# Kernel tuning notes

Measured on AMD Instinct MI355X. Metric: run time of the kernel, lower is better.

## Reference

```python
import jax, jax.numpy as jnp
import numpy as np
from jax import lax

T, K, D = 2097152, 8, 4
LOG_2PI = float(np.log(2.0 * np.pi))


def setup_inputs() -> dict:
    key = jax.random.key(0)
    k1, k2, k3, k4 = jax.random.split(key, 4)
    return {
        "x_seq": jax.random.normal(k1, (T, D), dtype=jnp.float32),
        "unnormalized_trans": jax.random.normal(k2, (K, K), dtype=jnp.float32),
        "unnormalized_pi": jax.random.normal(k3, (K,), dtype=jnp.float32),
        "means": jax.random.normal(k4, (K, D), dtype=jnp.float32) * 0.01,
        "log_std": jnp.zeros((K, D), dtype=jnp.float32),
    }


def reference(x_seq, unnormalized_trans, unnormalized_pi, means, log_std):
    # Row-stochastic transition / initial distributions in log space
    log_trans = jax.nn.log_softmax(unnormalized_trans, axis=-1)  # [K, K]
    log_pi = jax.nn.log_softmax(unnormalized_pi, axis=-1)        # [K]

    # Diagonal-Gaussian log emission densities: [T, K]
    std = jnp.exp(log_std)                                        # [K, D]
    z = (x_seq[:, None, :] - means[None, :, :]) / std[None, :, :]  # [T, K, D]
    log_em = jnp.sum(-0.5 * LOG_2PI - log_std[None] - 0.5 * z * z, axis=-1)  # [T, K]

    # Forward algorithm in log space (strictly sequential recurrence)
    alpha0 = log_pi + log_em[0]  # [K]

    def step(alpha, em_t):
        # alpha[i] + log_trans[i, j], logsumexp over source state i
        alpha = em_t + jax.scipy.special.logsumexp(alpha[:, None] + log_trans, axis=0)
        return alpha, None

    alpha, _ = lax.scan(step, alpha0, log_em[1:])
    return jax.scipy.special.logsumexp(alpha, axis=0)
```

## Files before the change

### kernel.cpp

```cpp
#include <hip/hip_runtime.h>
#include <math.h>

#define T_LEN 2097152
#define K 8
#define D 4
#define CHUNK 8
#define TPB 256
#define NBLK (T_LEN / (CHUNK * TPB))
#define MS4 19
#define NMID 8

typedef float f2 __attribute__((ext_vector_type(2)));

__device__ __forceinline__ f2 fma2(f2 a, f2 b, f2 c) { return __builtin_elementwise_fma(a, b, c); }
__device__ __forceinline__ f2 max2(f2 a, f2 b) { return __builtin_elementwise_max(a, b); }
__device__ __forceinline__ f2 splat(float s) { f2 r; r.x = s; r.y = s; return r; }


__device__ __forceinline__ float4* matp4(float* lm, int li) {
    return reinterpret_cast<float4*>(lm) + li * MS4 + ((li >> 1) & 3);
}

__device__ __forceinline__ void renorm2(f2 M[K][4], float& shift) {
    f2 m2 = max2(max2(M[0][0], M[0][1]), max2(M[0][2], M[0][3]));
#pragma unroll
    for (int i = 1; i < K; ++i)
        m2 = max2(m2, max2(max2(M[i][0], M[i][1]), max2(M[i][2], M[i][3])));
    float mx = fmaxf(m2.x, m2.y);
    int ex = (__float_as_int(mx) >> 23) & 255;
    float scale = __int_as_float((254 - ex) << 23);
    shift += (float)(ex - 127);
    f2 sc = splat(scale);
#pragma unroll
    for (int i = 0; i < K; ++i)
#pragma unroll
        for (int jj = 0; jj < 4; ++jj) M[i][jj] = M[i][jj] * sc;
}

__device__ __forceinline__ void store_mat(float* lm, int li, const f2 M[K][4]) {
    float4* dst = matp4(lm, li);
#pragma unroll
    for (int i = 0; i < K; ++i) {
        float4 w0, w1;
        w0.x = M[i][0].x; w0.y = M[i][0].y; w0.z = M[i][1].x; w0.w = M[i][1].y;
        w1.x = M[i][2].x; w1.y = M[i][2].y; w1.z = M[i][3].x; w1.w = M[i][3].y;
        dst[i * 2] = w0;
        dst[i * 2 + 1] = w1;
    }
}

__device__ __forceinline__ void combine8(float* lm, float* lsh, int li, int ri, int i) {
    const float4* Lb = matp4(lm, li);
    const float4* Rb = matp4(lm, ri);
    float4 la = Lb[i * 2], lb = Lb[i * 2 + 1];
    float4 R[16];
#pragma unroll
    for (int q = 0; q < 16; ++q) R[q] = Rb[q];
    float lk[8] = {la.x, la.y, la.z, la.w, lb.x, lb.y, lb.z, lb.w};
    f2 acc[4];
#pragma unroll
    for (int k = 0; k < 8; ++k) {
        f2 s = splat(lk[k]);
        f2 r0, r1, r2_, r3;
        r0.x = R[2 * k].x;     r0.y = R[2 * k].y;
        r1.x = R[2 * k].z;     r1.y = R[2 * k].w;
        r2_.x = R[2 * k + 1].x; r2_.y = R[2 * k + 1].y;
        r3.x = R[2 * k + 1].z;  r3.y = R[2 * k + 1].w;
        if (k == 0) {
            acc[0] = s * r0; acc[1] = s * r1; acc[2] = s * r2_; acc[3] = s * r3;
        } else {
            acc[0] = fma2(s, r0, acc[0]); acc[1] = fma2(s, r1, acc[1]);
            acc[2] = fma2(s, r2_, acc[2]); acc[3] = fma2(s, r3, acc[3]);
        }
    }
    f2 m2 = max2(max2(acc[0], acc[1]), max2(acc[2], acc[3]));
    float mx = fmaxf(m2.x, m2.y);
    mx = fmaxf(mx, __shfl_xor(mx, 1));
    mx = fmaxf(mx, __shfl_xor(mx, 2));
    mx = fmaxf(mx, __shfl_xor(mx, 4));
    int ex = (__float_as_int(mx) >> 23) & 255;
    float scale = __int_as_float((254 - ex) << 23);
    float ns = lsh[li] + lsh[ri] + (float)(ex - 127);
    f2 sc = splat(scale);
    f2 o0 = acc[0] * sc, o1 = acc[1] * sc, o2 = acc[2] * sc, o3 = acc[3] * sc;
    float4 w0, w1;
    w0.x = o0.x; w0.y = o0.y; w0.z = o1.x; w0.w = o1.y;
    w1.x = o2.x; w1.y = o2.y; w1.z = o3.x; w1.w = o3.y;
    float4* Ob = matp4(lm, li);
    Ob[i * 2] = w0;
    Ob[i * 2 + 1] = w1;
    if (i == 0) lsh[li] = ns;
}

__device__ __forceinline__ void tree_levels(float* lm, float* lsh) {
    const int g = threadIdx.x >> 3;
    const int i = threadIdx.x & 7;
#pragma unroll 1
    for (int lvl = 1; lvl <= 3; ++lvl) {
        const int c = 64 >> (lvl - 1);
        const int S = 1 << (lvl - 1);
#pragma unroll 1
        for (int m = g; m < c; m += 32) combine8(lm, lsh, 2 * m * S, 2 * m * S + S, i);
        __syncthreads();
    }
    if (threadIdx.x < 64) {
#pragma unroll 1
        for (int lvl = 4; lvl <= 7; ++lvl) {
            const int c = 64 >> (lvl - 1);
            const int S = 1 << (lvl - 1);
            if (g < c) combine8(lm, lsh, 2 * g * S, 2 * g * S + S, i);
            asm volatile("s_waitcnt lgkmcnt(0)" ::: "memory");
        }
    }
}

__device__ __forceinline__ void hybrid_tree(f2 P2[K][4], float shift, float* lm, float* lsh) {
    const int t = threadIdx.x;
    if ((t & 1) == 0) {
        store_mat(lm, t >> 1, P2);
        lsh[t >> 1] = shift;
    }
    __syncthreads();
    if (t & 1) {
        const float4* src = matp4(lm, t >> 1);
        float lsv = lsh[t >> 1];
        f2 C[K][4];
#pragma unroll
        for (int i = 0; i < K; ++i) {
            float4 la = src[i * 2], lb = src[i * 2 + 1];
            float lk[8] = {la.x, la.y, la.z, la.w, lb.x, lb.y, lb.z, lb.w};
            f2 q[4];
#pragma unroll
            for (int k = 0; k < 8; ++k) {
                f2 s = splat(lk[k]);
                if (k == 0) {
#pragma unroll
                    for (int jj = 0; jj < 4; ++jj) q[jj] = s * P2[k][jj];
                } else {
#pragma unroll
                    for (int jj = 0; jj < 4; ++jj) q[jj] = fma2(s, P2[k][jj], q[jj]);
                }
            }
#pragma unroll
            for (int jj = 0; jj < 4; ++jj) C[i][jj] = q[jj];
        }
        float ns = shift + lsv;
        renorm2(C, ns);
        store_mat(lm, t >> 1, C);
        lsh[t >> 1] = ns;
    }
    __syncthreads();
    tree_levels(lm, lsh);
}

__device__ __forceinline__ float emit_e2(const f2 ca2[4], const f2 cb2[4][4],
                                         const f2 cc2[4][4], float4 x, f2 e2[4]) {
    f2 x0 = splat(x.x), x1 = splat(x.y), x2 = splat(x.z), x3 = splat(x.w);
    f2 em2[4];
#pragma unroll
    for (int jj = 0; jj < 4; ++jj) {
        f2 t = ca2[jj];
        t = fma2(fma2(cc2[0][jj], x0, cb2[0][jj]), x0, t);
        t = fma2(fma2(cc2[1][jj], x1, cb2[1][jj]), x1, t);
        t = fma2(fma2(cc2[2][jj], x2, cb2[2][jj]), x2, t);
        t = fma2(fma2(cc2[3][jj], x3, cb2[3][jj]), x3, t);
        em2[jj] = t;
    }
    f2 m2 = max2(max2(em2[0], em2[1]), max2(em2[2], em2[3]));
    float me = fmaxf(m2.x, m2.y);
#pragma unroll
    for (int jj = 0; jj < 4; ++jj) {
        e2[jj].x = exp2f(em2[jj].x - me);
        e2[jj].y = exp2f(em2[jj].y - me);
    }
    return me;
}

__global__ void hmm_setup(const float* __restrict__ x,
                          const float* __restrict__ ut,
                          const float* __restrict__ up,
                          const float* __restrict__ mn,
                          const float* __restrict__ lsd,
                          float* __restrict__ ws) {
    const int lane = threadIdx.x;
    const float L2PI = 1.83787706640934548356f;
    const float LOG2E = 1.44269504088896340736f;

    float v = ut[lane];
    float m = v;
    m = fmaxf(m, __shfl_xor(m, 1));
    m = fmaxf(m, __shfl_xor(m, 2));
    m = fmaxf(m, __shfl_xor(m, 4));
    float e = expf(v - m);
    float s = e;
    s += __shfl_xor(s, 1); s += __shfl_xor(s, 2); s += __shfl_xor(s, 4);
    ws[lane] = e / s;

    float pv = up[lane & 7];
    float pm = pv;
    pm = fmaxf(pm, __shfl_xor(pm, 1));
    pm = fmaxf(pm, __shfl_xor(pm, 2));
    pm = fmaxf(pm, __shfl_xor(pm, 4));
    float pe = expf(pv - pm);
    float ps = pe;
    ps += __shfl_xor(ps, 1); ps += __shfl_xor(ps, 2); ps += __shfl_xor(ps, 4);
    float pival = pe / ps;

    int k = (lane & 31) >> 2, d = lane & 3;
    float lv = lsd[k * D + d];
    float mu = mn[k * D + d];
    float iv = expf(-2.f * lv);
    float bn = mu * iv;
    float cn = -0.5f * iv;
    float aterm = -0.5f * L2PI - lv - 0.5f * mu * mu * iv;
    float ak = aterm;
    ak += __shfl_xor(ak, 1); ak += __shfl_xor(ak, 2);
    if (lane < 32) {
        ws[72 + lane]  = bn * LOG2E;
        ws[104 + lane] = cn * LOG2E;
        if (d == 0) ws[64 + k] = ak * LOG2E;
    }

    float xd = x[d];
    float part = (cn * xd + bn) * xd + aterm;
    part += __shfl_xor(part, 1); part += __shfl_xor(part, 2);
    float pik = __shfl(pival, k);
    if (lane < 32 && d == 0) ws[136 + k] = pik * expf(part);
}

__global__ __launch_bounds__(TPB) void hmm_main(const float* __restrict__ x,
                                                const float* __restrict__ cst,
                                                float* __restrict__ bp,
                                                float* __restrict__ bs) {
    __shared__ __align__(16) float lm[128 * 76];
    __shared__ float lsh[128];
    const int tid = blockIdx.x * TPB + threadIdx.x;

    float Tr[K][K];
#pragma unroll
    for (int i = 0; i < K; ++i)
#pragma unroll
        for (int j = 0; j < K; ++j) Tr[i][j] = cst[i * K + j];
    f2 Tr2[K][4];
#pragma unroll
    for (int i = 0; i < K; ++i)
#pragma unroll
        for (int jj = 0; jj < 4; ++jj) { Tr2[i][jj].x = Tr[i][2 * jj]; Tr2[i][jj].y = Tr[i][2 * jj + 1]; }

    f2 ca2[4], cb2[4][4], cc2[4][4];
#pragma unroll
    for (int jj = 0; jj < 4; ++jj) {
        ca2[jj].x = cst[64 + 2 * jj]; ca2[jj].y = cst[64 + 2 * jj + 1];
#pragma unroll
        for (int d = 0; d < 4; ++d) {
            cb2[d][jj].x = cst[72 + (2 * jj) * 4 + d];  cb2[d][jj].y = cst[72 + (2 * jj + 1) * 4 + d];
            cc2[d][jj].x = cst[104 + (2 * jj) * 4 + d]; cc2[d][jj].y = cst[104 + (2 * jj + 1) * 4 + d];
        }
    }

    const float4* xv = reinterpret_cast<const float4*>(x) + (size_t)tid * CHUNK;
    float4 xr[CHUNK];
#pragma unroll
    for (int t = 0; t < CHUNK; ++t) xr[t] = xv[t];

    f2 T2[K][4];
    float shift;
    {
        f2 eB[4];
        float meB = emit_e2(ca2, cb2, cc2, xr[1], eB);
        if (tid == 0) {
#pragma unroll
            for (int i = 0; i < K; ++i) {
                f2 a0 = splat(cst[136 + i]);
#pragma unroll
                for (int jj = 0; jj < 4; ++jj) T2[i][jj] = a0 * Tr2[i][jj] * eB[jj];
            }
            shift = meB;
        } else {
            f2 eA[4];
            float meA = emit_e2(ca2, cb2, cc2, xr[0], eA);
#pragma unroll
            for (int i = 0; i < K; ++i) {
                f2 ei = splat((i & 1) ? eA[i >> 1].y : eA[i >> 1].x);
#pragma unroll
                for (int jj = 0; jj < 4; ++jj) T2[i][jj] = ei * Tr2[i][jj] * eB[jj];
            }
            shift = meA + meB;
        }
    }

#pragma unroll
    for (int p = 1; p < 4; ++p) {
        f2 eA[4], eB[4];
        float meA = emit_e2(ca2, cb2, cc2, xr[2 * p], eA);
        float meB = emit_e2(ca2, cb2, cc2, xr[2 * p + 1], eB);
        shift += meA + meB;
#pragma unroll
        for (int i = 0; i < K; ++i) {
            f2 r2[4];
#pragma unroll
            for (int kk = 0; kk < 4; ++kk) r2[kk] = T2[i][kk] * eA[kk];
            f2 u[4];
#pragma unroll
            for (int jj = 0; jj < 4; ++jj) u[jj] = splat(r2[0].x) * Tr2[0][jj];
#pragma unroll
            for (int k = 1; k < 8; ++k) {
                f2 rk = splat((k & 1) ? r2[k >> 1].y : r2[k >> 1].x);
#pragma unroll
                for (int jj = 0; jj < 4; ++jj) u[jj] = fma2(rk, Tr2[k][jj], u[jj]);
            }
#pragma unroll
            for (int jj = 0; jj < 4; ++jj) T2[i][jj] = u[jj] * eB[jj];
        }
    }

    if (tid != 0) {
#pragma unroll
        for (int jj = 0; jj < 4; ++jj) {
            f2 c[K];
#pragma unroll
            for (int k = 0; k < K; ++k) c[k] = T2[k][jj];
#pragma unroll
            for (int i = 0; i < K; ++i) {
                f2 a = splat(Tr[i][0]) * c[0];
#pragma unroll
                for (int k = 1; k < K; ++k) a = fma2(splat(Tr[i][k]), c[k], a);
                T2[i][jj] = a;
            }
        }
    }

    renorm2(T2, shift);

    hybrid_tree(T2, shift, lm, lsh);

    if (threadIdx.x == 0) {
        float4* o4 = reinterpret_cast<float4*>(bp + (size_t)blockIdx.x * 64);
        const float4* l4 = reinterpret_cast<const float4*>(lm);
#pragma unroll
        for (int q = 0; q < 16; ++q) o4[q] = l4[q];
        bs[blockIdx.x] = lsh[0];
    }
}

__global__ __launch_bounds__(TPB) void hmm_mid(const float* __restrict__ bp,
                                               const float* __restrict__ bs,
                                               float* __restrict__ bp2,
                                               float* __restrict__ bs2) {
    __shared__ __align__(16) float lm[128 * 76];
    __shared__ float lsh[128];
    const int t = threadIdx.x;
    const int m = t >> 1;
    const int h = t & 1;
    const int gbase = blockIdx.x * 128;

    {
        const float4* src = reinterpret_cast<const float4*>(bp + (size_t)(gbase + m) * 64) + h * 8;
        float4 v[8];
#pragma unroll
        for (int q = 0; q < 8; ++q) v[q] = src[q];
        float4* dst = matp4(lm, m) + h * 8;
#pragma unroll
        for (int q = 0; q < 8; ++q) dst[q] = v[q];
    }
    if (t < 128) lsh[t] = bs[gbase + t];
    __syncthreads();

    tree_levels(lm, lsh);

    if (t == 0) {
        float4* o4 = reinterpret_cast<float4*>(bp2 + (size_t)blockIdx.x * 64);
        const float4* l4 = reinterpret_cast<const float4*>(lm);
#pragma unroll
        for (int q = 0; q < 16; ++q) o4[q] = l4[q];
        bs2[blockIdx.x] = lsh[0];
    }
}

__global__ __launch_bounds__(64) void hmm_final(const float* __restrict__ bp2,
                                                const float* __restrict__ bs2,
                                                float* __restrict__ out) {
    __shared__ __align__(16) float lm[8 * 76];
    __shared__ float lsh[8];
    const int t = threadIdx.x;
    const int g = t >> 3;
    const int i = t & 7;

    {
        const float4* src = reinterpret_cast<const float4*>(bp2 + (size_t)g * 64) + i * 2;
        float4 a = src[0], b = src[1];
        float4* dst = matp4(lm, g) + i * 2;
        dst[0] = a; dst[1] = b;
    }
    if (i == 0) lsh[g] = bs2[g];
    __syncthreads();

    if (g < 4) combine8(lm, lsh, 2 * g, 2 * g + 1, i);
    __syncthreads();
    if (g < 2) combine8(lm, lsh, 4 * g, 4 * g + 2, i);
    __syncthreads();
    if (g < 1) combine8(lm, lsh, 0, 4, i);
    __syncthreads();

    if (t == 0) {
        double s = 0.0;
#pragma unroll
        for (int q = 0; q < 64; ++q) s += (double)lm[q];
        out[0] = (float)(log(s) + (double)lsh[0] * 0.69314718055994530942);
    }
}

extern "C" void kernel_launch(void* const* d_in, const int* in_sizes, int n_in,
                              void* d_out, int out_size, void* d_ws, size_t ws_size,
                              hipStream_t stream) {
    (void)in_sizes; (void)n_in; (void)out_size; (void)ws_size;
    const float* x  = (const float*)d_in[0];
    const float* ut = (const float*)d_in[1];
    const float* up = (const float*)d_in[2];
    const float* mn = (const float*)d_in[3];
    const float* ls = (const float*)d_in[4];
    float* ws  = (float*)d_ws;
    float* out = (float*)d_out;
    float* bp  = ws + 256;
    float* bs  = bp + (size_t)NBLK * 64;
    float* bp2 = bs + NBLK;
    float* bs2 = bp2 + (size_t)NMID * 64;

    hmm_setup<<<1, 64, 0, stream>>>(x, ut, up, mn, ls, ws);
    hmm_main<<<NBLK, TPB, 0, stream>>>(x, ws, bp, bs);
    hmm_mid<<<NMID, TPB, 0, stream>>>(bp, bs, bp2, bs2);
    hmm_final<<<1, 64, 0, stream>>>(bp2, bs2, out);
}
```

Before: 121.4 us.

## Shrink main blocks to 64 threads and fuse final reduction into mid via ticket

The main kernel now runs 64-thread blocks with a smaller shared-memory tree, giving four times as many blocks, each doing a shallower reduction. The mid kernel now takes one 8x8 matrix per thread into registers, uses the hybrid 256 tree, and the last block to finish (found through an atomic ticket counter) performs the final combine. This removes one kernel launch and the deep single-block tree levels that ran with only 64 active threads. The cost is more partial matrices written to global memory and an added atomic counter that the setup kernel must reset on every call.

```diff
diff --git a/kernel.cpp b/kernel.cpp
--- a/kernel.cpp
+++ b/kernel.cpp
@@ -5,10 +5,11 @@
 #define K 8
 #define D 4
 #define CHUNK 8
-#define TPB 256
+#define TPB 64
 #define NBLK (T_LEN / (CHUNK * TPB))
 #define MS4 19
-#define NMID 8
+#define NMID 16
+#define MPM (NBLK / NMID)
 
 typedef float f2 __attribute__((ext_vector_type(2)));
 
@@ -62,8 +63,8 @@
     for (int k = 0; k < 8; ++k) {
         f2 s = splat(lk[k]);
         f2 r0, r1, r2_, r3;
-        r0.x = R[2 * k].x;     r0.y = R[2 * k].y;
-        r1.x = R[2 * k].z;     r1.y = R[2 * k].w;
+        r0.x = R[2 * k].x;      r0.y = R[2 * k].y;
+        r1.x = R[2 * k].z;      r1.y = R[2 * k].w;
         r2_.x = R[2 * k + 1].x; r2_.y = R[2 * k + 1].y;
         r3.x = R[2 * k + 1].z;  r3.y = R[2 * k + 1].w;
         if (k == 0) {
@@ -92,7 +93,58 @@
     if (i == 0) lsh[li] = ns;
 }
 
-__device__ __forceinline__ void tree_levels(float* lm, float* lsh) {
+__device__ __forceinline__ void hybrid_tree64(f2 P2[K][4], float shift, float* lm, float* lsh) {
+    const int t = threadIdx.x;
+    const int g = t >> 3;
+    const int i = t & 7;
+    if ((t & 1) == 0) {
+        store_mat(lm, t >> 1, P2);
+        lsh[t >> 1] = shift;
+    }
+    __syncthreads();
+    if (t & 1) {
+        const float4* src = matp4(lm, t >> 1);
+        float lsv = lsh[t >> 1];
+        f2 C[K][4];
+#pragma unroll
+        for (int r = 0; r < K; ++r) {
+            float4 la = src[r * 2], lb = src[r * 2 + 1];
+            float lk[8] = {la.x, la.y, la.z, la.w, lb.x, lb.y, lb.z, lb.w};
+            f2 q[4];
+#pragma unroll
+            for (int k = 0; k < 8; ++k) {
+                f2 s = splat(lk[k]);
+                if (k == 0) {
+#pragma unroll
+                    for (int jj = 0; jj < 4; ++jj) q[jj] = s * P2[k][jj];
+                } else {
+#pragma unroll
+                    for (int jj = 0; jj < 4; ++jj) q[jj] = fma2(s, P2[k][jj], q[jj]);
+                }
+            }
+#pragma unroll
+            for (int jj = 0; jj < 4; ++jj) C[r][jj] = q[jj];
+        }
+        float ns = shift + lsv;
+        renorm2(C, ns);
+        store_mat(lm, t >> 1, C);
+        lsh[t >> 1] = ns;
+    }
+    __syncthreads();
+    combine8(lm, lsh, 2 * g, 2 * g + 1, i);
+    combine8(lm, lsh, 2 * (g + 8), 2 * (g + 8) + 1, i);
+    __syncthreads();
+    combine8(lm, lsh, 4 * g, 4 * g + 2, i);
+    __syncthreads();
+    if (g < 4) combine8(lm, lsh, 8 * g, 8 * g + 4, i);
+    __syncthreads();
+    if (g < 2) combine8(lm, lsh, 16 * g, 16 * g + 8, i);
+    __syncthreads();
+    if (g < 1) combine8(lm, lsh, 0, 16, i);
+    __syncthreads();
+}
+
+__device__ __forceinline__ void tree_levels256(float* lm, float* lsh) {
     const int g = threadIdx.x >> 3;
     const int i = threadIdx.x & 7;
 #pragma unroll 1
@@ -114,7 +166,7 @@
     }
 }
 
-__device__ __forceinline__ void hybrid_tree(f2 P2[K][4], float shift, float* lm, float* lsh) {
+__device__ __forceinline__ void hybrid_tree256(f2 P2[K][4], float shift, float* lm, float* lsh) {
     const int t = threadIdx.x;
     if ((t & 1) == 0) {
         store_mat(lm, t >> 1, P2);
@@ -126,8 +178,8 @@
         float lsv = lsh[t >> 1];
         f2 C[K][4];
 #pragma unroll
-        for (int i = 0; i < K; ++i) {
-            float4 la = src[i * 2], lb = src[i * 2 + 1];
+        for (int r = 0; r < K; ++r) {
+            float4 la = src[r * 2], lb = src[r * 2 + 1];
             float lk[8] = {la.x, la.y, la.z, la.w, lb.x, lb.y, lb.z, lb.w};
             f2 q[4];
 #pragma unroll
@@ -142,7 +194,7 @@
                 }
             }
 #pragma unroll
-            for (int jj = 0; jj < 4; ++jj) C[i][jj] = q[jj];
+            for (int jj = 0; jj < 4; ++jj) C[r][jj] = q[jj];
         }
         float ns = shift + lsv;
         renorm2(C, ns);
@@ -150,7 +202,7 @@
         lsh[t >> 1] = ns;
     }
     __syncthreads();
-    tree_levels(lm, lsh);
+    tree_levels256(lm, lsh);
 }
 
 __device__ __forceinline__ float emit_e2(const f2 ca2[4], const f2 cb2[4][4],
@@ -185,6 +237,8 @@
     const int lane = threadIdx.x;
     const float L2PI = 1.83787706640934548356f;
     const float LOG2E = 1.44269504088896340736f;
+
+    if (lane == 0) reinterpret_cast<unsigned*>(ws + 152)[0] = 0u;
 
     float v = ut[lane];
     float m = v;
@@ -232,8 +286,8 @@
                                                 const float* __restrict__ cst,
                                                 float* __restrict__ bp,
                                                 float* __restrict__ bs) {
-    __shared__ __align__(16) float lm[128 * 76];
-    __shared__ float lsh[128];
+    __shared__ __align__(16) float lm[32 * 76];
+    __shared__ float lsh[32];
     const int tid = blockIdx.x * TPB + threadIdx.x;
 
     float Tr[K][K];
@@ -332,7 +386,7 @@
 
     renorm2(T2, shift);
 
-    hybrid_tree(T2, shift, lm, lsh);
+    hybrid_tree64(T2, shift, lm, lsh);
 
     if (threadIdx.x == 0) {
         float4* o4 = reinterpret_cast<float4*>(bp + (size_t)blockIdx.x * 64);
@@ -343,63 +397,64 @@
     }
 }
 
-__global__ __launch_bounds__(TPB) void hmm_mid(const float* __restrict__ bp,
+__global__ __launch_bounds__(256) void hmm_mid(const float* __restrict__ bp,
                                                const float* __restrict__ bs,
                                                float* __restrict__ bp2,
-                                               float* __restrict__ bs2) {
+                                               float* __restrict__ bs2,
+                                               unsigned* __restrict__ cnt,
+                                               float* __restrict__ out) {
     __shared__ __align__(16) float lm[128 * 76];
     __shared__ float lsh[128];
+    __shared__ int lastflag;
     const int t = threadIdx.x;
-    const int m = t >> 1;
-    const int h = t & 1;
-    const int gbase = blockIdx.x * 128;
-
+    const int g8 = t >> 3, i8 = t & 7;
+
+    f2 P2[K][4];
     {
-        const float4* src = reinterpret_cast<const float4*>(bp + (size_t)(gbase + m) * 64) + h * 8;
-        float4 v[8];
-#pragma unroll
-        for (int q = 0; q < 8; ++q) v[q] = src[q];
-        float4* dst = matp4(lm, m) + h * 8;
-#pragma unroll
-        for (int q = 0; q < 8; ++q) dst[q] = v[q];
-    }
-    if (t < 128) lsh[t] = bs[gbase + t];
-    __syncthreads();
-
-    tree_levels(lm, lsh);
+        const float4* p4 = reinterpret_cast<const float4*>(bp + (size_t)(blockIdx.x * MPM + t) * 64);
+#pragma unroll
+        for (int r = 0; r < K; ++r) {
+            float4 a = p4[2 * r], b = p4[2 * r + 1];
+            P2[r][0].x = a.x; P2[r][0].y = a.y;
+            P2[r][1].x = a.z; P2[r][1].y = a.w;
+            P2[r][2].x = b.x; P2[r][2].y = b.y;
+            P2[r][3].x = b.z; P2[r][3].y = b.w;
+        }
+    }
+    float shift = bs[blockIdx.x * MPM + t];
+
+    hybrid_tree256(P2, shift, lm, lsh);
 
     if (t == 0) {
-        float4* o4 = reinterpret_cast<float4*>(bp2 + (size_t)blockIdx.x * 64);
-        const float4* l4 = reinterpret_cast<const float4*>(lm);
-#pragma unroll
-        for (int q = 0; q < 16; ++q) o4[q] = l4[q];
-        bs2[blockIdx.x] = lsh[0];
-    }
-}
-
-__global__ __launch_bounds__(64) void hmm_final(const float* __restrict__ bp2,
-                                                const float* __restrict__ bs2,
-                                                float* __restrict__ out) {
-    __shared__ __align__(16) float lm[8 * 76];
-    __shared__ float lsh[8];
-    const int t = threadIdx.x;
-    const int g = t >> 3;
-    const int i = t & 7;
-
-    {
-        const float4* src = reinterpret_cast<const float4*>(bp2 + (size_t)g * 64) + i * 2;
-        float4 a = src[0], b = src[1];
-        float4* dst = matp4(lm, g) + i * 2;
-        dst[0] = a; dst[1] = b;
-    }
-    if (i == 0) lsh[g] = bs2[g];
-    __syncthreads();
-
-    if (g < 4) combine8(lm, lsh, 2 * g, 2 * g + 1, i);
-    __syncthreads();
-    if (g < 2) combine8(lm, lsh, 4 * g, 4 * g + 2, i);
-    __syncthreads();
-    if (g < 1) combine8(lm, lsh, 0, 4, i);
+        const float* l0 = lm;
+#pragma unroll
+        for (int q = 0; q < 64; ++q)
+            __hip_atomic_store(&bp2[blockIdx.x * 64 + q], l0[q], __ATOMIC_RELAXED, __HIP_MEMORY_SCOPE_AGENT);
+        __hip_atomic_store(&bs2[blockIdx.x], lsh[0], __ATOMIC_RELAXED, __HIP_MEMORY_SCOPE_AGENT);
+        __threadfence();
+        unsigned ticket = __hip_atomic_fetch_add(cnt, 1u, __ATOMIC_ACQ_REL, __HIP_MEMORY_SCOPE_AGENT);
+        lastflag = (ticket == NMID - 1) ? 1 : 0;
+    }
+    __syncthreads();
+    if (!lastflag) return;
+
+    __threadfence();
+    if (t < 128) {
+        const int g = t >> 3, i = t & 7;
+        float* rowp = reinterpret_cast<float*>(matp4(lm, g) + 2 * i);
+#pragma unroll
+        for (int c = 0; c < 8; ++c)
+            rowp[c] = __hip_atomic_load(&bp2[g * 64 + i * 8 + c], __ATOMIC_RELAXED, __HIP_MEMORY_SCOPE_AGENT);
+        if (i == 0) lsh[g] = __hip_atomic_load(&bs2[g], __ATOMIC_RELAXED, __HIP_MEMORY_SCOPE_AGENT);
+    }
+    __syncthreads();
+    if (t < 64) combine8(lm, lsh, 2 * g8, 2 * g8 + 1, i8);
+    __syncthreads();
+    if (t < 32) combine8(lm, lsh, 4 * g8, 4 * g8 + 2, i8);
+    __syncthreads();
+    if (t < 16) combine8(lm, lsh, 8 * g8, 8 * g8 + 4, i8);
+    __syncthreads();
+    if (t < 8)  combine8(lm, lsh, 0, 8, i8);
     __syncthreads();
 
     if (t == 0) {
@@ -425,9 +480,9 @@
     float* bs  = bp + (size_t)NBLK * 64;
     float* bp2 = bs + NBLK;
     float* bs2 = bp2 + (size_t)NMID * 64;
+    unsigned* cnt = reinterpret_cast<unsigned*>(ws + 152);
 
     hmm_setup<<<1, 64, 0, stream>>>(x, ut, up, mn, ls, ws);
     hmm_main<<<NBLK, TPB, 0, stream>>>(x, ws, bp, bs);
-    hmm_mid<<<NMID, TPB, 0, stream>>>(bp, bs, bp2, bs2);
-    hmm_final<<<1, 64, 0, stream>>>(bp2, bs2, out);
-}
+    hmm_mid<<<NMID, 256, 0, stream>>>(bp, bs, bp2, bs2, cnt, out);
+}
```

After: 126.4 us. 1.04x slower.

## Fuse mid and final tree reductions into main kernel via last-block atomic counters

Applied to the files above, without the earlier changes.

Shrinks the main kernel blocks to 64 threads and replaces the separate mid and final reduction kernels with a last-block-done scheme. Per-group atomic counters let the last block of each 64-block group combine the group's matrices, and a global counter lets the last group reducer produce the final output. This removes two kernel launches and their launch gaps. In exchange it adds atomics, fences, agent-scope loads and smaller blocks with more per-block overhead.

```diff
diff --git a/kernel.cpp b/kernel.cpp
--- a/kernel.cpp
+++ b/kernel.cpp
@@ -5,10 +5,11 @@
 #define K 8
 #define D 4
 #define CHUNK 8
-#define TPB 256
+#define TPB 64
 #define NBLK (T_LEN / (CHUNK * TPB))
 #define MS4 19
-#define NMID 8
+#define GRP 64
+#define NGRP (NBLK / GRP)
 
 typedef float f2 __attribute__((ext_vector_type(2)));
 
@@ -62,8 +63,8 @@
     for (int k = 0; k < 8; ++k) {
         f2 s = splat(lk[k]);
         f2 r0, r1, r2_, r3;
-        r0.x = R[2 * k].x;     r0.y = R[2 * k].y;
-        r1.x = R[2 * k].z;     r1.y = R[2 * k].w;
+        r0.x = R[2 * k].x;      r0.y = R[2 * k].y;
+        r1.x = R[2 * k].z;      r1.y = R[2 * k].w;
         r2_.x = R[2 * k + 1].x; r2_.y = R[2 * k + 1].y;
         r3.x = R[2 * k + 1].z;  r3.y = R[2 * k + 1].w;
         if (k == 0) {
@@ -92,30 +93,10 @@
     if (i == 0) lsh[li] = ns;
 }
 
-__device__ __forceinline__ void tree_levels(float* lm, float* lsh) {
-    const int g = threadIdx.x >> 3;
-    const int i = threadIdx.x & 7;
-#pragma unroll 1
-    for (int lvl = 1; lvl <= 3; ++lvl) {
-        const int c = 64 >> (lvl - 1);
-        const int S = 1 << (lvl - 1);
-#pragma unroll 1
-        for (int m = g; m < c; m += 32) combine8(lm, lsh, 2 * m * S, 2 * m * S + S, i);
-        __syncthreads();
-    }
-    if (threadIdx.x < 64) {
-#pragma unroll 1
-        for (int lvl = 4; lvl <= 7; ++lvl) {
-            const int c = 64 >> (lvl - 1);
-            const int S = 1 << (lvl - 1);
-            if (g < c) combine8(lm, lsh, 2 * g * S, 2 * g * S + S, i);
-            asm volatile("s_waitcnt lgkmcnt(0)" ::: "memory");
-        }
-    }
-}
-
-__device__ __forceinline__ void hybrid_tree(f2 P2[K][4], float shift, float* lm, float* lsh) {
+__device__ __forceinline__ void hybrid_tree64(f2 P2[K][4], float shift, float* lm, float* lsh) {
     const int t = threadIdx.x;
+    const int g = t >> 3;
+    const int i = t & 7;
     if ((t & 1) == 0) {
         store_mat(lm, t >> 1, P2);
         lsh[t >> 1] = shift;
@@ -126,8 +107,8 @@
         float lsv = lsh[t >> 1];
         f2 C[K][4];
 #pragma unroll
-        for (int i = 0; i < K; ++i) {
-            float4 la = src[i * 2], lb = src[i * 2 + 1];
+        for (int r = 0; r < K; ++r) {
+            float4 la = src[r * 2], lb = src[r * 2 + 1];
             float lk[8] = {la.x, la.y, la.z, la.w, lb.x, lb.y, lb.z, lb.w};
             f2 q[4];
 #pragma unroll
@@ -142,7 +123,7 @@
                 }
             }
 #pragma unroll
-            for (int jj = 0; jj < 4; ++jj) C[i][jj] = q[jj];
+            for (int jj = 0; jj < 4; ++jj) C[r][jj] = q[jj];
         }
         float ns = shift + lsv;
         renorm2(C, ns);
@@ -150,7 +131,30 @@
         lsh[t >> 1] = ns;
     }
     __syncthreads();
-    tree_levels(lm, lsh);
+    combine8(lm, lsh, 2 * g, 2 * g + 1, i);
+    combine8(lm, lsh, 2 * (g + 8), 2 * (g + 8) + 1, i);
+    __syncthreads();
+    combine8(lm, lsh, 4 * g, 4 * g + 2, i);
+    __syncthreads();
+    if (g < 4) combine8(lm, lsh, 8 * g, 8 * g + 4, i);
+    __syncthreads();
+    if (g < 2) combine8(lm, lsh, 16 * g, 16 * g + 8, i);
+    __syncthreads();
+    if (g < 1) combine8(lm, lsh, 0, 16, i);
+    __syncthreads();
+}
+
+__device__ __forceinline__ float load_mat_agent(const float* __restrict__ p, const float* __restrict__ ps,
+                                                int m, f2 P2[K][4]) {
+    float v[64];
+#pragma unroll
+    for (int q = 0; q < 64; ++q)
+        v[q] = __hip_atomic_load(&p[(size_t)m * 64 + q], __ATOMIC_RELAXED, __HIP_MEMORY_SCOPE_AGENT);
+#pragma unroll
+    for (int r = 0; r < K; ++r)
+#pragma unroll
+        for (int jj = 0; jj < 4; ++jj) { P2[r][jj].x = v[r * 8 + 2 * jj]; P2[r][jj].y = v[r * 8 + 2 * jj + 1]; }
+    return __hip_atomic_load(&ps[m], __ATOMIC_RELAXED, __HIP_MEMORY_SCOPE_AGENT);
 }
 
 __device__ __forceinline__ float emit_e2(const f2 ca2[4], const f2 cb2[4][4],
@@ -185,6 +189,9 @@
     const int lane = threadIdx.x;
     const float L2PI = 1.83787706640934548356f;
     const float LOG2E = 1.44269504088896340736f;
+
+    reinterpret_cast<unsigned*>(ws + 160)[lane] = 0u;
+    if (lane == 0) reinterpret_cast<unsigned*>(ws + 152)[0] = 0u;
 
     float v = ut[lane];
     float m = v;
@@ -231,10 +238,18 @@
 __global__ __launch_bounds__(TPB) void hmm_main(const float* __restrict__ x,
                                                 const float* __restrict__ cst,
                                                 float* __restrict__ bp,
-                                                float* __restrict__ bs) {
-    __shared__ __align__(16) float lm[128 * 76];
-    __shared__ float lsh[128];
-    const int tid = blockIdx.x * TPB + threadIdx.x;
+                                                float* __restrict__ bs,
+                                                float* __restrict__ gp,
+                                                float* __restrict__ gs,
+                                                unsigned* __restrict__ gc,
+                                                unsigned* __restrict__ gcnt,
+                                                float* __restrict__ out) {
+    __shared__ __align__(16) float lm[32 * 76];
+    __shared__ float lsh[32];
+    __shared__ int flag;
+    const int t = threadIdx.x;
+    const int tid = blockIdx.x * TPB + t;
+    const int grp = blockIdx.x >> 6;
 
     float Tr[K][K];
 #pragma unroll
@@ -261,7 +276,7 @@
     const float4* xv = reinterpret_cast<const float4*>(x) + (size_t)tid * CHUNK;
     float4 xr[CHUNK];
 #pragma unroll
-    for (int t = 0; t < CHUNK; ++t) xr[t] = xv[t];
+    for (int q = 0; q < CHUNK; ++q) xr[q] = xv[q];
 
     f2 T2[K][4];
     float shift;
@@ -332,76 +347,40 @@
 
     renorm2(T2, shift);
 
-    hybrid_tree(T2, shift, lm, lsh);
-
-    if (threadIdx.x == 0) {
-        float4* o4 = reinterpret_cast<float4*>(bp + (size_t)blockIdx.x * 64);
-        const float4* l4 = reinterpret_cast<const float4*>(lm);
-#pragma unroll
-        for (int q = 0; q < 16; ++q) o4[q] = l4[q];
-        bs[blockIdx.x] = lsh[0];
-    }
-}
-
-__global__ __launch_bounds__(TPB) void hmm_mid(const float* __restrict__ bp,
-                                               const float* __restrict__ bs,
-                                               float* __restrict__ bp2,
-                                               float* __restrict__ bs2) {
-    __shared__ __align__(16) float lm[128 * 76];
-    __shared__ float lsh[128];
-    const int t = threadIdx.x;
-    const int m = t >> 1;
-    const int h = t & 1;
-    const int gbase = blockIdx.x * 128;
-
+    hybrid_tree64(T2, shift, lm, lsh);
+
+    __hip_atomic_store(&bp[(size_t)blockIdx.x * 64 + t], lm[t], __ATOMIC_RELAXED, __HIP_MEMORY_SCOPE_AGENT);
+    if (t == 0) {
+        __hip_atomic_store(&bs[blockIdx.x], lsh[0], __ATOMIC_RELAXED, __HIP_MEMORY_SCOPE_AGENT);
+        __threadfence();
+        unsigned tk = __hip_atomic_fetch_add(&gc[grp], 1u, __ATOMIC_ACQ_REL, __HIP_MEMORY_SCOPE_AGENT);
+        flag = (tk == GRP - 1) ? 1 : 0;
+    }
+    __syncthreads();
+    if (!flag) return;
+
+    __threadfence();
     {
-        const float4* src = reinterpret_cast<const float4*>(bp + (size_t)(gbase + m) * 64) + h * 8;
-        float4 v[8];
-#pragma unroll
-        for (int q = 0; q < 8; ++q) v[q] = src[q];
-        float4* dst = matp4(lm, m) + h * 8;
-#pragma unroll
-        for (int q = 0; q < 8; ++q) dst[q] = v[q];
-    }
-    if (t < 128) lsh[t] = bs[gbase + t];
-    __syncthreads();
-
-    tree_levels(lm, lsh);
-
+        f2 P2[K][4];
+        float sh = load_mat_agent(bp, bs, grp * GRP + t, P2);
+        hybrid_tree64(P2, sh, lm, lsh);
+    }
+    __hip_atomic_store(&gp[(size_t)grp * 64 + t], lm[t], __ATOMIC_RELAXED, __HIP_MEMORY_SCOPE_AGENT);
     if (t == 0) {
-        float4* o4 = reinterpret_cast<float4*>(bp2 + (size_t)blockIdx.x * 64);
-        const float4* l4 = reinterpret_cast<const float4*>(lm);
-#pragma unroll
-        for (int q = 0; q < 16; ++q) o4[q] = l4[q];
-        bs2[blockIdx.x] = lsh[0];
-    }
-}
-
-__global__ __launch_bounds__(64) void hmm_final(const float* __restrict__ bp2,
-                                                const float* __restrict__ bs2,
-                                                float* __restrict__ out) {
-    __shared__ __align__(16) float lm[8 * 76];
-    __shared__ float lsh[8];
-    const int t = threadIdx.x;
-    const int g = t >> 3;
-    const int i = t & 7;
-
+        __hip_atomic_store(&gs[grp], lsh[0], __ATOMIC_RELAXED, __HIP_MEMORY_SCOPE_AGENT);
+        __threadfence();
+        unsigned tk = __hip_atomic_fetch_add(gcnt, 1u, __ATOMIC_ACQ_REL, __HIP_MEMORY_SCOPE_AGENT);
+        flag = (tk == NGRP - 1) ? 1 : 0;
+    }
+    __syncthreads();
+    if (!flag) return;
+
+    __threadfence();
     {
-        const float4* src = reinterpret_cast<const float4*>(bp2 + (size_t)g * 64) + i * 2;
-        float4 a = src[0], b = src[1];
-        float4* dst = matp4(lm, g) + i * 2;
-        dst[0] = a; dst[1] = b;
-    }
-    if (i == 0) lsh[g] = bs2[g];
-    __syncthreads();
-
-    if (g < 4) combine8(lm, lsh, 2 * g, 2 * g + 1, i);
-    __syncthreads();
-    if (g < 2) combine8(lm, lsh, 4 * g, 4 * g + 2, i);
-    __syncthreads();
-    if (g < 1) combine8(lm, lsh, 0, 4, i);
-    __syncthreads();
-
+        f2 P2[K][4];
+        float sh = load_mat_agent(gp, gs, t, P2);
+        hybrid_tree64(P2, sh, lm, lsh);
+    }
     if (t == 0) {
         double s = 0.0;
 #pragma unroll
@@ -423,11 +402,11 @@
     float* out = (float*)d_out;
     float* bp  = ws + 256;
     float* bs  = bp + (size_t)NBLK * 64;
-    float* bp2 = bs + NBLK;
-    float* bs2 = bp2 + (size_t)NMID * 64;
+    float* gp  = bs + NBLK;
+    float* gs  = gp + (size_t)NGRP * 64;
+    unsigned* gcnt = reinterpret_cast<unsigned*>(ws + 152);
+    unsigned* gc   = reinterpret_cast<unsigned*>(ws + 160);
 
     hmm_setup<<<1, 64, 0, stream>>>(x, ut, up, mn, ls, ws);
-    hmm_main<<<NBLK, TPB, 0, stream>>>(x, ws, bp, bs);
-    hmm_mid<<<NMID, TPB, 0, stream>>>(bp, bs, bp2, bs2);
-    hmm_final<<<1, 64, 0, stream>>>(bp2, bs2, out);
-}
+    hmm_main<<<NBLK, TPB, 0, stream>>>(x, ws, bp, bs, gp, gs, gc, gcnt, out);
+}
```

Measured after the change: 247.4 us. +103.9%, slower.

## Shrink main-kernel blocks to one wavefront and widen the mid/final reduction tree

Applied to the files above, without the earlier changes.

The main kernel now runs 64-thread blocks, so each block reduces only 64 chunk matrices in a shallower tree of 5 combine levels, with less shared memory and fewer block-wide barriers. NBLK grows fourfold, so the mid stage uses 32 blocks of 128 matrices each, and the final kernel combines 32 partial products with 128 threads. The block result is written out by all 64 threads in parallel instead of by thread 0 alone. The intent is to shorten the serial tail of the in-block tree and raise occupancy. The cost is more global partial matrices and a deeper final combine.

```diff
diff --git a/kernel.cpp b/kernel.cpp
--- a/kernel.cpp
+++ b/kernel.cpp
@@ -5,10 +5,11 @@
 #define K 8
 #define D 4
 #define CHUNK 8
-#define TPB 256
+#define TPB 64
 #define NBLK (T_LEN / (CHUNK * TPB))
 #define MS4 19
-#define NMID 8
+#define NMID 32
+#define MPM (NBLK / NMID)
 
 typedef float f2 __attribute__((ext_vector_type(2)));
 
@@ -62,8 +63,8 @@
     for (int k = 0; k < 8; ++k) {
         f2 s = splat(lk[k]);
         f2 r0, r1, r2_, r3;
-        r0.x = R[2 * k].x;     r0.y = R[2 * k].y;
-        r1.x = R[2 * k].z;     r1.y = R[2 * k].w;
+        r0.x = R[2 * k].x;      r0.y = R[2 * k].y;
+        r1.x = R[2 * k].z;      r1.y = R[2 * k].w;
         r2_.x = R[2 * k + 1].x; r2_.y = R[2 * k + 1].y;
         r3.x = R[2 * k + 1].z;  r3.y = R[2 * k + 1].w;
         if (k == 0) {
@@ -92,7 +93,58 @@
     if (i == 0) lsh[li] = ns;
 }
 
-__device__ __forceinline__ void tree_levels(float* lm, float* lsh) {
+__device__ __forceinline__ void hybrid_tree64(f2 P2[K][4], float shift, float* lm, float* lsh) {
+    const int t = threadIdx.x;
+    const int g = t >> 3;
+    const int i = t & 7;
+    if ((t & 1) == 0) {
+        store_mat(lm, t >> 1, P2);
+        lsh[t >> 1] = shift;
+    }
+    __syncthreads();
+    if (t & 1) {
+        const float4* src = matp4(lm, t >> 1);
+        float lsv = lsh[t >> 1];
+        f2 C[K][4];
+#pragma unroll
+        for (int r = 0; r < K; ++r) {
+            float4 la = src[r * 2], lb = src[r * 2 + 1];
+            float lk[8] = {la.x, la.y, la.z, la.w, lb.x, lb.y, lb.z, lb.w};
+            f2 q[4];
+#pragma unroll
+            for (int k = 0; k < 8; ++k) {
+                f2 s = splat(lk[k]);
+                if (k == 0) {
+#pragma unroll
+                    for (int jj = 0; jj < 4; ++jj) q[jj] = s * P2[k][jj];
+                } else {
+#pragma unroll
+                    for (int jj = 0; jj < 4; ++jj) q[jj] = fma2(s, P2[k][jj], q[jj]);
+                }
+            }
+#pragma unroll
+            for (int jj = 0; jj < 4; ++jj) C[r][jj] = q[jj];
+        }
+        float ns = shift + lsv;
+        renorm2(C, ns);
+        store_mat(lm, t >> 1, C);
+        lsh[t >> 1] = ns;
+    }
+    __syncthreads();
+    combine8(lm, lsh, 2 * g, 2 * g + 1, i);
+    combine8(lm, lsh, 2 * (g + 8), 2 * (g + 8) + 1, i);
+    __syncthreads();
+    combine8(lm, lsh, 4 * g, 4 * g + 2, i);
+    __syncthreads();
+    if (g < 4) combine8(lm, lsh, 8 * g, 8 * g + 4, i);
+    __syncthreads();
+    if (g < 2) combine8(lm, lsh, 16 * g, 16 * g + 8, i);
+    __syncthreads();
+    if (g < 1) combine8(lm, lsh, 0, 16, i);
+    __syncthreads();
+}
+
+__device__ __forceinline__ void tree_levels256(float* lm, float* lsh) {
     const int g = threadIdx.x >> 3;
     const int i = threadIdx.x & 7;
 #pragma unroll 1
@@ -112,45 +164,6 @@
             asm volatile("s_waitcnt lgkmcnt(0)" ::: "memory");
         }
     }
-}
-
-__device__ __forceinline__ void hybrid_tree(f2 P2[K][4], float shift, float* lm, float* lsh) {
-    const int t = threadIdx.x;
-    if ((t & 1) == 0) {
-        store_mat(lm, t >> 1, P2);
-        lsh[t >> 1] = shift;
-    }
-    __syncthreads();
-    if (t & 1) {
-        const float4* src = matp4(lm, t >> 1);
-        float lsv = lsh[t >> 1];
-        f2 C[K][4];
-#pragma unroll
-        for (int i = 0; i < K; ++i) {
-            float4 la = src[i * 2], lb = src[i * 2 + 1];
-            float lk[8] = {la.x, la.y, la.z, la.w, lb.x, lb.y, lb.z, lb.w};
-            f2 q[4];
-#pragma unroll
-            for (int k = 0; k < 8; ++k) {
-                f2 s = splat(lk[k]);
-                if (k == 0) {
-#pragma unroll
-                    for (int jj = 0; jj < 4; ++jj) q[jj] = s * P2[k][jj];
-                } else {
-#pragma unroll
-                    for (int jj = 0; jj < 4; ++jj) q[jj] = fma2(s, P2[k][jj], q[jj]);
-                }
-            }
-#pragma unroll
-            for (int jj = 0; jj < 4; ++jj) C[i][jj] = q[jj];
-        }
-        float ns = shift + lsv;
-        renorm2(C, ns);
-        store_mat(lm, t >> 1, C);
-        lsh[t >> 1] = ns;
-    }
-    __syncthreads();
-    tree_levels(lm, lsh);
 }
 
 __device__ __forceinline__ float emit_e2(const f2 ca2[4], const f2 cb2[4][4],
@@ -232,9 +245,10 @@
                                                 const float* __restrict__ cst,
                                                 float* __restrict__ bp,
                                                 float* __restrict__ bs) {
-    __shared__ __align__(16) float lm[128 * 76];
-    __shared__ float lsh[128];
-    const int tid = blockIdx.x * TPB + threadIdx.x;
+    __shared__ __align__(16) float lm[32 * 76];
+    __shared__ float lsh[32];
+    const int t = threadIdx.x;
+    const int tid = blockIdx.x * TPB + t;
 
     float Tr[K][K];
 #pragma unroll
@@ -261,7 +275,7 @@
     const float4* xv = reinterpret_cast<const float4*>(x) + (size_t)tid * CHUNK;
     float4 xr[CHUNK];
 #pragma unroll
-    for (int t = 0; t < CHUNK; ++t) xr[t] = xv[t];
+    for (int q = 0; q < CHUNK; ++q) xr[q] = xv[q];
 
     f2 T2[K][4];
     float shift;
@@ -332,18 +346,13 @@
 
     renorm2(T2, shift);
 
-    hybrid_tree(T2, shift, lm, lsh);
-
-    if (threadIdx.x == 0) {
-        float4* o4 = reinterpret_cast<float4*>(bp + (size_t)blockIdx.x * 64);
-        const float4* l4 = reinterpret_cast<const float4*>(lm);
-#pragma unroll
-        for (int q = 0; q < 16; ++q) o4[q] = l4[q];
-        bs[blockIdx.x] = lsh[0];
-    }
-}
-
-__global__ __launch_bounds__(TPB) void hmm_mid(const float* __restrict__ bp,
+    hybrid_tree64(T2, shift, lm, lsh);
+
+    bp[(size_t)blockIdx.x * 64 + t] = lm[t];
+    if (t == 0) bs[blockIdx.x] = lsh[0];
+}
+
+__global__ __launch_bounds__(256) void hmm_mid(const float* __restrict__ bp,
                                                const float* __restrict__ bs,
                                                float* __restrict__ bp2,
                                                float* __restrict__ bs2) {
@@ -352,7 +361,7 @@
     const int t = threadIdx.x;
     const int m = t >> 1;
     const int h = t & 1;
-    const int gbase = blockIdx.x * 128;
+    const int gbase = blockIdx.x * MPM;
 
     {
         const float4* src = reinterpret_cast<const float4*>(bp + (size_t)(gbase + m) * 64) + h * 8;
@@ -366,7 +375,7 @@
     if (t < 128) lsh[t] = bs[gbase + t];
     __syncthreads();
 
-    tree_levels(lm, lsh);
+    tree_levels256(lm, lsh);
 
     if (t == 0) {
         float4* o4 = reinterpret_cast<float4*>(bp2 + (size_t)blockIdx.x * 64);
@@ -377,29 +386,36 @@
     }
 }
 
-__global__ __launch_bounds__(64) void hmm_final(const float* __restrict__ bp2,
-                                                const float* __restrict__ bs2,
-                                                float* __restrict__ out) {
-    __shared__ __align__(16) float lm[8 * 76];
-    __shared__ float lsh[8];
+__global__ __launch_bounds__(128) void hmm_final(const float* __restrict__ bp2,
+                                                 const float* __restrict__ bs2,
+                                                 float* __restrict__ out) {
+    __shared__ __align__(16) float lm[32 * 76];
+    __shared__ float lsh[32];
     const int t = threadIdx.x;
     const int g = t >> 3;
     const int i = t & 7;
 
     {
-        const float4* src = reinterpret_cast<const float4*>(bp2 + (size_t)g * 64) + i * 2;
-        float4 a = src[0], b = src[1];
-        float4* dst = matp4(lm, g) + i * 2;
-        dst[0] = a; dst[1] = b;
-    }
-    if (i == 0) lsh[g] = bs2[g];
-    __syncthreads();
-
-    if (g < 4) combine8(lm, lsh, 2 * g, 2 * g + 1, i);
-    __syncthreads();
-    if (g < 2) combine8(lm, lsh, 4 * g, 4 * g + 2, i);
-    __syncthreads();
-    if (g < 1) combine8(lm, lsh, 0, 4, i);
+        const float4* src = reinterpret_cast<const float4*>(bp2);
+#pragma unroll
+        for (int j = 0; j < 4; ++j) {
+            int f = t * 4 + j;
+            int mat = f >> 4, off = f & 15;
+            matp4(lm, mat)[off] = src[f];
+        }
+    }
+    if (t < 32) lsh[t] = bs2[t];
+    __syncthreads();
+
+    combine8(lm, lsh, 2 * g, 2 * g + 1, i);
+    __syncthreads();
+    if (g < 8) combine8(lm, lsh, 4 * g, 4 * g + 2, i);
+    __syncthreads();
+    if (g < 4) combine8(lm, lsh, 8 * g, 8 * g + 4, i);
+    __syncthreads();
+    if (g < 2) combine8(lm, lsh, 16 * g, 16 * g + 8, i);
+    __syncthreads();
+    if (g < 1) combine8(lm, lsh, 0, 16, i);
     __syncthreads();
 
     if (t == 0) {
@@ -428,6 +444,6 @@
 
     hmm_setup<<<1, 64, 0, stream>>>(x, ut, up, mn, ls, ws);
     hmm_main<<<NBLK, TPB, 0, stream>>>(x, ws, bp, bs);
-    hmm_mid<<<NMID, TPB, 0, stream>>>(bp, bs, bp2, bs2);
-    hmm_final<<<1, 64, 0, stream>>>(bp2, bs2, out);
-}
+    hmm_mid<<<NMID, 256, 0, stream>>>(bp, bs, bp2, bs2);
+    hmm_final<<<1, 128, 0, stream>>>(bp2, bs2, out);
+}
```

Result: no change. 119.3 us (-1.7%).
